# Optimization experiments

Measured on AMD Instinct MI355X. Metric: run time of the kernel, lower is better.

The kernel has to match this reference:

```python
import jax, jax.numpy as jnp
import numpy as np

EPS = 1e-06


def _create_circular_masks(h, w):
    # Faithful to the torch code: y spans width, x spans height -> mask shape (w, h).
    # Only used with square feature maps (h == w), matching the module's implicit assumption.
    cen_w, cen_h = w // 2, h // 2
    y = np.arange(-cen_w, w - cen_w).reshape(-1, 1)
    x = np.arange(-cen_h, h - cen_h).reshape(1, -1)
    y2, x2 = y * y, x * x
    r2 = x2 + y2
    masks = [r2 <= 0]
    max_r = int(np.sqrt(r2.max())) + 1
    quadrants = [(1, 1), (-1, 1), (1, -1), (-1, -1)]  # (sign_x, sign_y)
    for radius in range(1, max_r):
        lo, hi = (radius - 1) ** 2, radius ** 2
        for sx, sy in quadrants:
            quad = (sx * x >= 0) & (sy * y >= 0)
            masks.append((r2 > lo) & (r2 <= hi) & quad)  # ring mask
            masks.append((r2 <= hi) & quad)              # circle mask
    return np.stack(masks).astype(np.float32)  # [M, w, h] == [M, h, w] for square maps


def _l2_normalize(v):
    # v: [B, C]; torch norms over dim=1 with eps added to the norm
    return v / (jnp.linalg.norm(v, axis=1, keepdims=True) + EPS)


def setup_inputs() -> dict:
    key = jax.random.key(0)
    x = jax.random.normal(key, (32, 1024, 28, 28), dtype=jnp.float32)
    return {"x": x}


def reference(x) -> jnp.ndarray:
    B, C, H, W = x.shape
    masks = jnp.asarray(_create_circular_masks(H, W))  # [M, H, W] static constant
    # Global descriptor: max-pool over full map, then channel-wise L2 normalize.
    v = _l2_normalize(jnp.max(x, axis=(2, 3)))  # [B, C]
    # Accumulate masked-max descriptors; scan over the (fixed) mask set keeps
    # peak memory at one masked feature map instead of M of them.
    def step(acc, mask):
        vt = jnp.max(x * mask, axis=(2, 3))  # masked max-pool (zeros included, as in torch)
        return acc + _l2_normalize(vt), None
    v, _ = jax.lax.scan(step, v, masks)
    return v[:, :, None, None]  # [B, C, 1, 1] to match F.max_pool2d output shape
```

## Files before the change

### kernel.cpp

```cpp
#include <hip/hip_runtime.h>
#include <math.h>

#define B_DIM 32
#define C_DIM 1024
#define MAP 784
#define NMASK 153
#define NTERM 154
#define NROW 160
#define NBIN 77
#define DUMMY_BIN 77
#define MAX1 28
#define MAX2 6
#define MPW 2
#define NBLK 4096

struct Sched {
    unsigned short off1[MAX1][64];
    unsigned short off2[MAX2][64];
    unsigned char  binA[64];
    unsigned char  binB[64];
    bool ok;
};

constexpr Sched build_sched() {
    Sched S{};
    S.ok = true;
    short px[NBIN][40] = {};
    int   n[NBIN] = {};
    for (int i = 0; i < 28; ++i)
        for (int j = 0; j < 28; ++j) {
            int dy = i - 14, dx = j - 14, r2 = dx * dx + dy * dy;
            int p = i * 28 + j;
            if (r2 == 0) { px[0][n[0]++] = (short)p; continue; }
            if (r2 > 361) continue;
            int r = 0; while (r * r < r2) ++r;
            const int sx[4] = {1, -1, 1, -1}, sy[4] = {1, 1, -1, -1};
            for (int q = 0; q < 4; ++q)
                if (sx[q] * dx >= 0 && sy[q] * dy >= 0) {
                    int b = 1 + q * 19 + (r - 1);
                    if (n[b] >= 40) { S.ok = false; continue; }
                    px[b][n[b]++] = (short)p;
                }
        }
    int ord[NBIN] = {};
    for (int k = 0; k < NBIN; ++k) ord[k] = k;
    for (int a = 0; a < NBIN; ++a) {
        int best = a;
        for (int c = a + 1; c < NBIN; ++c)
            if (n[ord[c]] > n[ord[best]]) best = c;
        int t = ord[a]; ord[a] = ord[best]; ord[best] = t;
    }
    for (int l = 0; l < 64; ++l) {
        S.binA[l] = (unsigned char)ord[l];
        S.binB[l] = (l >= 51) ? (unsigned char)ord[64 + (l - 51)]
                              : (unsigned char)DUMMY_BIN;
        if (n[ord[l]] > MAX1) S.ok = false;
        if (l >= 51 && n[ord[64 + (l - 51)]] > MAX2) S.ok = false;
    }
    {
        bool used[64][40] = {};
        for (int s = 0; s < MAX1; ++s) {
            int bankcnt[32] = {};
            for (int l = 0; l < 64; ++l) {
                int bin = S.binA[l], cnt = n[bin];
                int bestp = 0, bestload = 1 << 30; bool haveUnused = false;
                for (int t = 0; t < cnt; ++t)
                    if (!used[l][t]) {
                        int load = bankcnt[px[bin][t] % 32];
                        if (!haveUnused || load < bestload) { haveUnused = true; bestload = load; bestp = t; }
                    }
                if (!haveUnused)
                    for (int t = 0; t < cnt; ++t) {
                        int load = bankcnt[px[bin][t] % 32];
                        if (load < bestload) { bestload = load; bestp = t; }
                    }
                int p = px[bin][bestp];
                if (haveUnused) used[l][bestp] = true;
                S.off1[s][l] = (unsigned short)(p * 4);
                bankcnt[p % 32]++;
            }
        }
        for (int l = 0; l < 64; ++l)
            for (int t = 0; t < n[S.binA[l]]; ++t)
                if (!used[l][t]) S.ok = false;
    }
    {
        bool used[64][40] = {};
        for (int s = 0; s < MAX2; ++s) {
            int bankcnt[32] = {};
            for (int l = 0; l < 64; ++l) {
                if (S.binB[l] == DUMMY_BIN) {
                    S.off2[s][l] = (unsigned short)((l % 32) * 4);
                    continue;
                }
                int bin = S.binB[l], cnt = n[bin];
                int bestp = 0, bestload = 1 << 30; bool haveUnused = false;
                for (int t = 0; t < cnt; ++t)
                    if (!used[l][t]) {
                        int load = bankcnt[px[bin][t] % 32];
                        if (!haveUnused || load < bestload) { haveUnused = true; bestload = load; bestp = t; }
                    }
                if (!haveUnused)
                    for (int t = 0; t < cnt; ++t) {
                        int load = bankcnt[px[bin][t] % 32];
                        if (load < bestload) { bestload = load; bestp = t; }
                    }
                int p = px[bin][bestp];
                if (haveUnused) used[l][bestp] = true;
                S.off2[s][l] = (unsigned short)(p * 4);
                bankcnt[p % 32]++;
            }
        }
        for (int l = 0; l < 64; ++l)
            if (S.binB[l] != DUMMY_BIN)
                for (int t = 0; t < n[S.binB[l]]; ++t)
                    if (!used[l][t]) S.ok = false;
    }
    return S;
}

static_assert(build_sched().ok, "schedule overflow / unplaced pixel");
__constant__ Sched d_sched = build_sched();

__device__ __forceinline__ int term_addr(int k) {
    if (k == 0) return 0;
    if (k >= NMASK) return DUMMY_BIN;
    int t = k - 1, q = (t >> 1) & 3, rm1 = t >> 3;
    return (t & 1) ? 78 + q * 19 + rm1
                   : 1 + q * 19 + rm1;
}

__global__ __launch_bounds__(256) void cac_k1(const float* __restrict__ x,
                                              float* __restrict__ vt,
                                              float* __restrict__ partial) {
    __shared__ __align__(16) float smap[4][MAP];
    __shared__ float sbuf[4][160];
    __shared__ float ssqred[4][NROW];

    const int wave = threadIdx.x >> 6;
    const int lane = threadIdx.x & 63;
    const int pair0 = blockIdx.x * (4 * MPW) + wave * MPW;

    const int linA = lane % 19;
    const bool inA = lane < 57, inB = lane < 19;
    const int rbA = 1 + lane;
    const int rbB = inB ? 58 + lane : DUMMY_BIN;
    const int a0 = term_addr(lane);
    const int a1 = term_addr(lane + 64);
    const int a2 = term_addr(lane + 128);

    const float4 NEG4 = make_float4(-INFINITY, -INFINITY, -INFINITY, -INFINITY);
    const float4* xp4 = (const float4*)(x + (size_t)pair0 * MAP);
    float4 t0 = xp4[lane], t1 = xp4[64 + lane], t2 = xp4[128 + lane];
    float4 t3 = NEG4;
    if (lane < 4) t3 = xp4[192 + lane];

    float* smw = smap[wave];
    float* sbw = sbuf[wave];
    float sq0 = 0.0f, sq1 = 0.0f, sq2 = 0.0f;

    #pragma unroll
    for (int m = 0; m < MPW; ++m) {
        ((float4*)smw)[lane]       = t0;
        ((float4*)smw)[64 + lane]  = t1;
        ((float4*)smw)[128 + lane] = t2;
        if (lane < 4) ((float4*)smw)[192 + lane] = t3;
        float gmax = fmaxf(fmaxf(fmaxf(t0.x, t0.y), fmaxf(t0.z, t0.w)),
                           fmaxf(fmaxf(t1.x, t1.y), fmaxf(t1.z, t1.w)));
        gmax = fmaxf(gmax, fmaxf(fmaxf(t2.x, t2.y), fmaxf(t2.z, t2.w)));
        gmax = fmaxf(gmax, fmaxf(fmaxf(t3.x, t3.y), fmaxf(t3.z, t3.w)));

        if (m < MPW - 1) {
            const float4* np4 = (const float4*)(x + (size_t)(pair0 + m + 1) * MAP);
            t0 = np4[lane]; t1 = np4[64 + lane]; t2 = np4[128 + lane];
            t3 = NEG4;
            if (lane < 4) t3 = np4[192 + lane];
        }
        __builtin_amdgcn_wave_barrier();

        const char* base = (const char*)smw;
        float m1 = 0.0f, m2v = 0.0f;
        #pragma unroll
        for (int s = 0; s < MAX1; ++s)
            m1 = fmaxf(m1, *(const float*)(base + d_sched.off1[s][lane]));
        #pragma unroll
        for (int s = 0; s < MAX2; ++s)
            m2v = fmaxf(m2v, *(const float*)(base + d_sched.off2[s][lane]));
        sbw[d_sched.binA[lane]] = m1;
        sbw[d_sched.binB[lane]] = m2v;

        #pragma unroll
        for (int off = 32; off; off >>= 1)
            gmax = fmaxf(gmax, __shfl_xor(gmax, off, 64));
        __builtin_amdgcn_wave_barrier();

        float cval = sbw[0];
        float rA = fmaxf(sbw[rbA], cval);
        float rB = fmaxf(sbw[rbB], cval);
        #pragma unroll
        for (int s = 1; s <= 16; s <<= 1) {
            float uA = __shfl_up(rA, s, 64);
            float uB = __shfl_up(rB, s, 64);
            if (linA >= s) rA = fmaxf(rA, uA);
            if (lane >= s) rB = fmaxf(rB, uB);
        }
        if (inA) sbw[78 + lane] = rA;
        if (inB) sbw[135 + lane] = rB;
        __builtin_amdgcn_wave_barrier();

        float r0 = sbw[a0];
        float r1 = sbw[a1];
        float r2 = sbw[a2];
        r2 = (lane == 25) ? gmax : (lane < 26 ? r2 : 0.0f);

        float* rowp = vt + (size_t)(pair0 + m) * NROW;
        rowp[lane]      = r0;
        rowp[64 + lane] = r1;
        if (lane < 32) rowp[128 + lane] = r2;
        sq0 += r0 * r0; sq1 += r1 * r1; sq2 += r2 * r2;
        __builtin_amdgcn_wave_barrier();
    }

    ssqred[wave][lane]      = sq0;
    ssqred[wave][64 + lane] = sq1;
    if (lane < 32) ssqred[wave][128 + lane] = sq2;
    __syncthreads();
    if (threadIdx.x < NROW) {
        int t = threadIdx.x;
        partial[(size_t)blockIdx.x * NROW + t] =
            ssqred[0][t] + ssqred[1][t] + ssqred[2][t] + ssqred[3][t];
    }
}

__global__ __launch_bounds__(256) void cac_k2(const float* __restrict__ vt,
                                              const float* __restrict__ partial,
                                              float* __restrict__ out) {
    __shared__ __align__(16) float sinv[NROW];
    const int b = blockIdx.x >> 3;

    if (threadIdx.x < NROW) {
        int t = threadIdx.x;
        const float* p = partial + (size_t)(b * 128) * NROW + t;
        float s = 0.0f;
        #pragma unroll 8
        for (int j = 0; j < 128; ++j) s += p[(size_t)j * NROW];
        sinv[t] = (t < NTERM) ? 1.0f / (sqrtf(s) + 1e-6f) : 0.0f;
    }
    __syncthreads();

    const int local = threadIdx.x >> 1;
    const int half  = threadIdx.x & 1;
    const int pair  = blockIdx.x * 128 + local;
    const float4* row = (const float4*)(vt + (size_t)pair * NROW + half * 80);
    const float4* w4  = (const float4*)(sinv + half * 80);
    float acc = 0.0f;
    #pragma unroll
    for (int i = 0; i < 20; ++i) {
        float4 v = row[i], w = w4[i];
        acc += v.x * w.x + v.y * w.y + v.z * w.z + v.w * w.w;
    }
    acc += __shfl_xor(acc, 1, 64);
    if (!half) out[pair] = acc;
}

extern "C" void kernel_launch(void* const* d_in, const int* in_sizes, int n_in,
                              void* d_out, int out_size, void* d_ws, size_t ws_size,
                              hipStream_t stream) {
    const float* x = (const float*)d_in[0];
    float* out = (float*)d_out;

    float* vt      = (float*)d_ws;
    float* partial = vt + (size_t)B_DIM * C_DIM * NROW;

    cac_k1<<<NBLK, 256, 0, stream>>>(x, vt, partial);
    cac_k2<<<256, 256, 0, stream>>>(vt, partial, out);
}
```

Before: 161.7 us.

## Fuse both kernels with a grid barrier and keep per-map terms in registers

Merges the masked-max kernel and the normalize/sum kernel into one persistent launch. Each wave now handles 8 maps instead of 2 and keeps its 160 terms per map in registers rather than writing them to a global vt buffer. A software grid barrier (atomic counter plus spin) waits until all per-block sum-of-squares partials are written, then each block applies the per-batch inverse norms itself. This removes the vt round-trip and the second launch, but it relies on all 1024 blocks being co-resident. It also adds a memset, barrier spin cost and more register pressure.

Measured after the change: 428.7 us. 2.65x slower.

```diff
diff --git a/kernel.cpp b/kernel.cpp
--- a/kernel.cpp
+++ b/kernel.cpp
@@ -11,8 +11,8 @@
 #define DUMMY_BIN 77
 #define MAX1 28
 #define MAX2 6
-#define MPW 2
-#define NBLK 4096
+#define MPW 8
+#define NBLK 1024
 
 struct Sched {
     unsigned short off1[MAX1][64];
@@ -130,16 +130,18 @@
                    : 1 + q * 19 + rm1;
 }
 
-__global__ __launch_bounds__(256) void cac_k1(const float* __restrict__ x,
-                                              float* __restrict__ vt,
-                                              float* __restrict__ partial) {
+__global__ __launch_bounds__(256, 4) void cac_fused(const float* __restrict__ x,
+                                                    float* __restrict__ partial,
+                                                    unsigned int* __restrict__ bar,
+                                                    float* __restrict__ out) {
     __shared__ __align__(16) float smap[4][MAP];
     __shared__ float sbuf[4][160];
     __shared__ float ssqred[4][NROW];
+    __shared__ float sinv[NROW];
 
     const int wave = threadIdx.x >> 6;
     const int lane = threadIdx.x & 63;
-    const int pair0 = blockIdx.x * (4 * MPW) + wave * MPW;
+    const int map0 = blockIdx.x * 32 + wave * MPW;
 
     const int linA = lane % 19;
     const bool inA = lane < 57, inB = lane < 19;
@@ -150,7 +152,7 @@
     const int a2 = term_addr(lane + 128);
 
     const float4 NEG4 = make_float4(-INFINITY, -INFINITY, -INFINITY, -INFINITY);
-    const float4* xp4 = (const float4*)(x + (size_t)pair0 * MAP);
+    const float4* xp4 = (const float4*)(x + (size_t)map0 * MAP);
     float4 t0 = xp4[lane], t1 = xp4[64 + lane], t2 = xp4[128 + lane];
     float4 t3 = NEG4;
     if (lane < 4) t3 = xp4[192 + lane];
@@ -158,6 +160,7 @@
     float* smw = smap[wave];
     float* sbw = sbuf[wave];
     float sq0 = 0.0f, sq1 = 0.0f, sq2 = 0.0f;
+    float rr0[MPW], rr1[MPW], rr2[MPW];
 
     #pragma unroll
     for (int m = 0; m < MPW; ++m) {
@@ -171,7 +174,7 @@
         gmax = fmaxf(gmax, fmaxf(fmaxf(t3.x, t3.y), fmaxf(t3.z, t3.w)));
 
         if (m < MPW - 1) {
-            const float4* np4 = (const float4*)(x + (size_t)(pair0 + m + 1) * MAP);
+            const float4* np4 = (const float4*)(x + (size_t)(map0 + m + 1) * MAP);
             t0 = np4[lane]; t1 = np4[64 + lane]; t2 = np4[128 + lane];
             t3 = NEG4;
             if (lane < 4) t3 = np4[192 + lane];
@@ -213,10 +216,7 @@
         float r2 = sbw[a2];
         r2 = (lane == 25) ? gmax : (lane < 26 ? r2 : 0.0f);
 
-        float* rowp = vt + (size_t)(pair0 + m) * NROW;
-        rowp[lane]      = r0;
-        rowp[64 + lane] = r1;
-        if (lane < 32) rowp[128 + lane] = r2;
+        rr0[m] = r0; rr1[m] = r1; rr2[m] = r2;
         sq0 += r0 * r0; sq1 += r1 * r1; sq2 += r2 * r2;
         __builtin_amdgcn_wave_barrier();
     }
@@ -230,37 +230,40 @@
         partial[(size_t)blockIdx.x * NROW + t] =
             ssqred[0][t] + ssqred[1][t] + ssqred[2][t] + ssqred[3][t];
     }
-}
-
-__global__ __launch_bounds__(256) void cac_k2(const float* __restrict__ vt,
-                                              const float* __restrict__ partial,
-                                              float* __restrict__ out) {
-    __shared__ __align__(16) float sinv[NROW];
-    const int b = blockIdx.x >> 3;
+
+    __threadfence();
+    __syncthreads();
+    if (threadIdx.x == 0) {
+        __hip_atomic_fetch_add(bar, 1u, __ATOMIC_ACQ_REL, __HIP_MEMORY_SCOPE_AGENT);
+        int budget = 1 << 20;
+        while (__hip_atomic_load(bar, __ATOMIC_RELAXED, __HIP_MEMORY_SCOPE_AGENT) < NBLK
+               && --budget)
+            __builtin_amdgcn_s_sleep(2);
+    }
+    __syncthreads();
+    __threadfence();
 
     if (threadIdx.x < NROW) {
         int t = threadIdx.x;
-        const float* p = partial + (size_t)(b * 128) * NROW + t;
+        const float* p = partial + (size_t)(blockIdx.x & ~31) * NROW + t;
         float s = 0.0f;
         #pragma unroll 8
-        for (int j = 0; j < 128; ++j) s += p[(size_t)j * NROW];
+        for (int j = 0; j < 32; ++j) s += p[(size_t)j * NROW];
         sinv[t] = (t < NTERM) ? 1.0f / (sqrtf(s) + 1e-6f) : 0.0f;
     }
     __syncthreads();
 
-    const int local = threadIdx.x >> 1;
-    const int half  = threadIdx.x & 1;
-    const int pair  = blockIdx.x * 128 + local;
-    const float4* row = (const float4*)(vt + (size_t)pair * NROW + half * 80);
-    const float4* w4  = (const float4*)(sinv + half * 80);
-    float acc = 0.0f;
+    const float sl0 = sinv[lane];
+    const float sl1 = sinv[64 + lane];
+    const float sl2 = (lane < 32) ? sinv[128 + lane] : 0.0f;
     #pragma unroll
-    for (int i = 0; i < 20; ++i) {
-        float4 v = row[i], w = w4[i];
-        acc += v.x * w.x + v.y * w.y + v.z * w.z + v.w * w.w;
-    }
-    acc += __shfl_xor(acc, 1, 64);
-    if (!half) out[pair] = acc;
+    for (int m = 0; m < MPW; ++m) {
+        float acc = rr0[m] * sl0 + rr1[m] * sl1 + rr2[m] * sl2;
+        #pragma unroll
+        for (int off = 32; off; off >>= 1)
+            acc += __shfl_xor(acc, off, 64);
+        if (lane == 0) out[map0 + m] = acc;
+    }
 }
 
 extern "C" void kernel_launch(void* const* d_in, const int* in_sizes, int n_in,
@@ -269,9 +272,10 @@
     const float* x = (const float*)d_in[0];
     float* out = (float*)d_out;
 
-    float* vt      = (float*)d_ws;
-    float* partial = vt + (size_t)B_DIM * C_DIM * NROW;
-
-    cac_k1<<<NBLK, 256, 0, stream>>>(x, vt, partial);
-    cac_k2<<<256, 256, 0, stream>>>(vt, partial, out);
-}
+    float* partial = (float*)d_ws;
+    unsigned int* bar = (unsigned int*)((char*)d_ws +
+                          (size_t)NBLK * NROW * sizeof(float));
+
+    hipMemsetAsync(bar, 0, 256, stream);
+    cac_fused<<<NBLK, 256, 0, stream>>>(x, partial, bar, out);
+}
```
